# Performance work log

Measured on AMD Instinct MI355X. Metric: run time of the kernel, lower is better.

The kernel has to match this reference:

```python
import jax, jax.numpy as jnp
import numpy as np

N = 100000      # number of nodes (z rows) and z0 rows
E = 1000000     # number of edges
EMB = 128       # args.emb_size


def setup_inputs() -> dict:
    key = jax.random.key(0)
    k1, k2, k3, k4, k5 = jax.random.split(key, 5)
    z = jax.random.normal(k1, (N, EMB), dtype=jnp.float32)
    z0 = jax.random.normal(k2, (N, EMB), dtype=jnp.float32)
    edge_index = jax.random.randint(k3, (2, E), 0, N, dtype=jnp.int64)
    # torch Linear weights: [out_features, in_features]
    Wq = jax.random.normal(k4, (EMB, 2 * EMB), dtype=jnp.float32) * (1.0 / np.sqrt(2 * EMB))
    Wo = jax.random.normal(k5, (1, 2 * EMB), dtype=jnp.float32) * (1.0 / np.sqrt(2 * EMB))
    bo = jnp.zeros((1,), dtype=jnp.float32)
    return {"z": z, "edge_index": edge_index, "z0": z0, "Wq": Wq, "Wo": Wo, "bo": bo}


def reference(z, edge_index, z0, Wq, Wo, bo):
    # qid: per-edge max of the two endpoint ids, shifted to start at 0
    qid = jnp.max(edge_index[0:2], axis=0)
    qid = qid - qid.min()
    emb1 = z[edge_index[0]]            # [E, EMB]
    emb2 = z[edge_index[1]]            # [E, EMB]
    x0 = jnp.concatenate([emb2, z0[qid]], axis=-1) @ Wq.T   # [E, EMB]
    out = jnp.concatenate([emb1, x0], axis=-1) @ Wo.T + bo  # [E, 1]
    return out.reshape(-1)
```

## Files before the change

kernel.cpp:

```cpp
#include <hip/hip_runtime.h>
#include <climits>

#define EMB 128
#define EMB2 256

__global__ void prep_weights_kernel(const float* __restrict__ Wq,
                                    const float* __restrict__ Wo,
                                    float* __restrict__ weff,
                                    int* __restrict__ qmin) {
    int k = threadIdx.x;
    float acc = 0.f;
#pragma unroll 8
    for (int j = 0; j < EMB; ++j)
        acc += Wo[EMB + j] * Wq[j * EMB2 + k];
    weff[k] = acc;
    if (k == 0) *qmin = INT_MAX;
}

__global__ void qmin_kernel(const int* __restrict__ ei, int E,
                            int* __restrict__ qmin) {
    int m = INT_MAX;
    int nvec = E >> 2;
    int stride = gridDim.x * blockDim.x;
    const int4* r0 = (const int4*)ei;
    const int4* r1 = (const int4*)(ei + E);
    for (int v = blockIdx.x * blockDim.x + threadIdx.x; v < nvec; v += stride) {
        int4 a = r0[v];
        int4 b = r1[v];
        int m0 = max(a.x, b.x), m1 = max(a.y, b.y);
        int m2 = max(a.z, b.z), m3 = max(a.w, b.w);
        m = min(m, min(min(m0, m1), min(m2, m3)));
    }
    if (blockIdx.x == 0 && threadIdx.x < (E & 3)) {
        int e = (nvec << 2) + threadIdx.x;
        m = min(m, max(ei[e], ei[e + E]));
    }
    for (int off = 32; off; off >>= 1)
        m = min(m, __shfl_xor(m, off, 64));
    __shared__ int sm[8];
    int wid = threadIdx.x >> 6;
    if ((threadIdx.x & 63) == 0) sm[wid] = m;
    __syncthreads();
    if (threadIdx.x == 0) {
        int nw = blockDim.x >> 6;
        int r = sm[0];
        for (int w = 1; w < nw; ++w) r = min(r, sm[w]);
        atomicMin(qmin, r);
    }
}

__global__ void node_dots_kernel(const float* __restrict__ z,
                                 const float* __restrict__ z0,
                                 const float* __restrict__ Wo,
                                 const float* __restrict__ weff,
                                 float4* __restrict__ tab,
                                 int N) {
    int gtid = blockIdx.x * blockDim.x + threadIdx.x;
    int wave = gtid >> 6;
    int lane = gtid & 63;
    int sub = lane >> 5;
    int c = lane & 31;
    int row = wave * 2 + sub;
    if (row >= N) return;

    float4 w1 = ((const float4*)Wo)[c];
    float4 wa = ((const float4*)weff)[c];
    float4 wb = ((const float4*)weff)[32 + c];

    float4 zv  = ((const float4*)(z  + (size_t)row * EMB))[c];
    float4 z0v = ((const float4*)(z0 + (size_t)row * EMB))[c];

    float p1 = w1.x * zv.x + w1.y * zv.y + w1.z * zv.z + w1.w * zv.w;
    float p2 = wa.x * zv.x + wa.y * zv.y + wa.z * zv.z + wa.w * zv.w;
    float p3 = wb.x * z0v.x + wb.y * z0v.y + wb.z * z0v.z + wb.w * z0v.w;

#pragma unroll
    for (int off = 16; off; off >>= 1) {
        p1 += __shfl_xor(p1, off, 64);
        p2 += __shfl_xor(p2, off, 64);
        p3 += __shfl_xor(p3, off, 64);
    }
    if (c == 0) tab[row] = make_float4(p1, p2, p3, 0.f);
}

__global__ void edge_out_kernel(const int* __restrict__ ei,
                                const float4* __restrict__ tab,
                                const int* __restrict__ qminp,
                                const float* __restrict__ bo,
                                float* __restrict__ out, int E) {
    int qmin = *qminp;
    float b0 = *bo;
    int t = blockIdx.x * blockDim.x + threadIdx.x;
    int e4 = t << 2;
    if (e4 + 3 < E) {
        int4 a = *(const int4*)(ei + e4);
        int4 b = *(const int4*)(ei + E + e4);
        float4 r;
        r.x = tab[a.x].x + tab[b.x].y + tab[max(a.x, b.x) - qmin].z + b0;
        r.y = tab[a.y].x + tab[b.y].y + tab[max(a.y, b.y) - qmin].z + b0;
        r.z = tab[a.z].x + tab[b.z].y + tab[max(a.z, b.z) - qmin].z + b0;
        r.w = tab[a.w].x + tab[b.w].y + tab[max(a.w, b.w) - qmin].z + b0;
        *(float4*)(out + e4) = r;
    } else {
        for (int e = e4; e < E; ++e) {
            int a = ei[e], b = ei[e + E];
            out[e] = tab[a].x + tab[b].y + tab[max(a, b) - qmin].z + b0;
        }
    }
}

extern "C" void kernel_launch(void* const* d_in, const int* in_sizes, int n_in,
                              void* d_out, int out_size, void* d_ws, size_t ws_size,
                              hipStream_t stream) {
    const float* z    = (const float*)d_in[0];
    const int*   ei   = (const int*)d_in[1];
    const float* z0   = (const float*)d_in[2];
    const float* Wq   = (const float*)d_in[3];
    const float* Wo   = (const float*)d_in[4];
    const float* bo   = (const float*)d_in[5];
    float* out = (float*)d_out;

    int N = in_sizes[0] / EMB;
    int E = in_sizes[1] / 2;

    float4* tab = (float4*)d_ws;
    float* weff = (float*)(tab + N);
    int*   qmin = (int*)(weff + EMB2);

    prep_weights_kernel<<<1, EMB2, 0, stream>>>(Wq, Wo, weff, qmin);

    qmin_kernel<<<512, 256, 0, stream>>>(ei, E, qmin);

    int pairs = (N + 1) / 2;
    int blocksC = (pairs + 3) / 4;
    node_dots_kernel<<<blocksC, 256, 0, stream>>>(z, z0, Wo, weff, tab, N);

    int threadsD = (E + 3) / 4;
    int blocksD = (threadsD + 255) / 256;
    edge_out_kernel<<<blocksD, 256, 0, stream>>>(ei, tab, qmin, bo, out, E);
}
```

Measured before the change: 158.6 us.

## Fuse qid-min scan into node dot-product kernel and use nontemporal loads/stores

```diff
diff --git a/kernel.cpp b/kernel.cpp
--- a/kernel.cpp
+++ b/kernel.cpp
@@ -4,10 +4,13 @@
 #define EMB 128
 #define EMB2 256
 
-__global__ void prep_weights_kernel(const float* __restrict__ Wq,
-                                    const float* __restrict__ Wo,
-                                    float* __restrict__ weff,
-                                    int* __restrict__ qmin) {
+typedef float v4f __attribute__((ext_vector_type(4)));
+typedef int   v4i __attribute__((ext_vector_type(4)));
+
+__global__ void weff_kernel(const float* __restrict__ Wq,
+                            const float* __restrict__ Wo,
+                            float* __restrict__ weff,
+                            int* __restrict__ qmin) {
     int k = threadIdx.x;
     float acc = 0.f;
 #pragma unroll 8
@@ -17,74 +20,78 @@
     if (k == 0) *qmin = INT_MAX;
 }
 
-__global__ void qmin_kernel(const int* __restrict__ ei, int E,
-                            int* __restrict__ qmin) {
-    int m = INT_MAX;
-    int nvec = E >> 2;
-    int stride = gridDim.x * blockDim.x;
-    const int4* r0 = (const int4*)ei;
-    const int4* r1 = (const int4*)(ei + E);
-    for (int v = blockIdx.x * blockDim.x + threadIdx.x; v < nvec; v += stride) {
-        int4 a = r0[v];
-        int4 b = r1[v];
-        int m0 = max(a.x, b.x), m1 = max(a.y, b.y);
-        int m2 = max(a.z, b.z), m3 = max(a.w, b.w);
-        m = min(m, min(min(m0, m1), min(m2, m3)));
-    }
-    if (blockIdx.x == 0 && threadIdx.x < (E & 3)) {
-        int e = (nvec << 2) + threadIdx.x;
-        m = min(m, max(ei[e], ei[e + E]));
-    }
-    for (int off = 32; off; off >>= 1)
-        m = min(m, __shfl_xor(m, off, 64));
-    __shared__ int sm[8];
-    int wid = threadIdx.x >> 6;
-    if ((threadIdx.x & 63) == 0) sm[wid] = m;
-    __syncthreads();
-    if (threadIdx.x == 0) {
-        int nw = blockDim.x >> 6;
-        int r = sm[0];
-        for (int w = 1; w < nw; ++w) r = min(r, sm[w]);
-        atomicMin(qmin, r);
-    }
-}
-
-__global__ void node_dots_kernel(const float* __restrict__ z,
+__global__ void scan_dots_kernel(const float* __restrict__ z,
                                  const float* __restrict__ z0,
+                                 const int* __restrict__ ei, int E,
                                  const float* __restrict__ Wo,
                                  const float* __restrict__ weff,
-                                 float4* __restrict__ tab,
-                                 int N) {
-    int gtid = blockIdx.x * blockDim.x + threadIdx.x;
-    int wave = gtid >> 6;
-    int lane = gtid & 63;
-    int sub = lane >> 5;
-    int c = lane & 31;
-    int row = wave * 2 + sub;
+                                 v4f* __restrict__ tab, int N,
+                                 int* __restrict__ qmin) {
+    const int gtid = blockIdx.x * blockDim.x + threadIdx.x;
+
+    {
+        int m = INT_MAX;
+        const int nvec = E >> 2;
+        if (gtid < nvec) {
+            v4i a = ((const v4i*)ei)[gtid];
+            v4i b = ((const v4i*)(ei + E))[gtid];
+            int m0 = max(a.x, b.x), m1 = max(a.y, b.y);
+            int m2 = max(a.z, b.z), m3 = max(a.w, b.w);
+            m = min(min(m0, m1), min(m2, m3));
+        }
+        if (gtid < (E & 3)) {
+            int e = (nvec << 2) + gtid;
+            m = min(m, max(ei[e], ei[e + E]));
+        }
+#pragma unroll
+        for (int off = 32; off; off >>= 1)
+            m = min(m, __shfl_xor(m, off, 64));
+        __shared__ int sm[4];
+        if ((threadIdx.x & 63) == 0) sm[threadIdx.x >> 6] = m;
+        __syncthreads();
+        if (threadIdx.x == 0)
+            atomicMin(qmin, min(min(sm[0], sm[1]), min(sm[2], sm[3])));
+    }
+
+    const int wave = gtid >> 6;
+    const int lane = gtid & 63;
+    const int sub = lane >> 4;
+    const int c = lane & 15;
+    const int row = wave * 4 + sub;
     if (row >= N) return;
 
-    float4 w1 = ((const float4*)Wo)[c];
-    float4 wa = ((const float4*)weff)[c];
-    float4 wb = ((const float4*)weff)[32 + c];
+    v4f w1a = ((const v4f*)Wo)[c],        w1b = ((const v4f*)Wo)[16 + c];
+    v4f waa = ((const v4f*)weff)[c],      wab = ((const v4f*)weff)[16 + c];
+    v4f wba = ((const v4f*)weff)[32 + c], wbb = ((const v4f*)weff)[48 + c];
 
-    float4 zv  = ((const float4*)(z  + (size_t)row * EMB))[c];
-    float4 z0v = ((const float4*)(z0 + (size_t)row * EMB))[c];
+    const v4f* zr  = (const v4f*)(z  + (size_t)row * EMB);
+    const v4f* z0r = (const v4f*)(z0 + (size_t)row * EMB);
+    v4f za = __builtin_nontemporal_load(zr + c);
+    v4f zb = __builtin_nontemporal_load(zr + 16 + c);
+    v4f qa = __builtin_nontemporal_load(z0r + c);
+    v4f qb = __builtin_nontemporal_load(z0r + 16 + c);
 
-    float p1 = w1.x * zv.x + w1.y * zv.y + w1.z * zv.z + w1.w * zv.w;
-    float p2 = wa.x * zv.x + wa.y * zv.y + wa.z * zv.z + wa.w * zv.w;
-    float p3 = wb.x * z0v.x + wb.y * z0v.y + wb.z * z0v.z + wb.w * z0v.w;
+    float p1 = w1a.x * za.x + w1a.y * za.y + w1a.z * za.z + w1a.w * za.w
+             + w1b.x * zb.x + w1b.y * zb.y + w1b.z * zb.z + w1b.w * zb.w;
+    float p2 = waa.x * za.x + waa.y * za.y + waa.z * za.z + waa.w * za.w
+             + wab.x * zb.x + wab.y * zb.y + wab.z * zb.z + wab.w * zb.w;
+    float p3 = wba.x * qa.x + wba.y * qa.y + wba.z * qa.z + wba.w * qa.w
+             + wbb.x * qb.x + wbb.y * qb.y + wbb.z * qb.z + wbb.w * qb.w;
 
 #pragma unroll
-    for (int off = 16; off; off >>= 1) {
+    for (int off = 8; off; off >>= 1) {
         p1 += __shfl_xor(p1, off, 64);
         p2 += __shfl_xor(p2, off, 64);
         p3 += __shfl_xor(p3, off, 64);
     }
-    if (c == 0) tab[row] = make_float4(p1, p2, p3, 0.f);
+    if (c == 0) {
+        v4f r; r.x = p1; r.y = p2; r.z = p3; r.w = 0.f;
+        tab[row] = r;
+    }
 }
 
 __global__ void edge_out_kernel(const int* __restrict__ ei,
-                                const float4* __restrict__ tab,
+                                const v4f* __restrict__ tab,
                                 const int* __restrict__ qminp,
                                 const float* __restrict__ bo,
                                 float* __restrict__ out, int E) {
@@ -93,14 +100,14 @@
     int t = blockIdx.x * blockDim.x + threadIdx.x;
     int e4 = t << 2;
     if (e4 + 3 < E) {
-        int4 a = *(const int4*)(ei + e4);
-        int4 b = *(const int4*)(ei + E + e4);
-        float4 r;
+        v4i a = *(const v4i*)(ei + e4);
+        v4i b = *(const v4i*)(ei + E + e4);
+        v4f r;
         r.x = tab[a.x].x + tab[b.x].y + tab[max(a.x, b.x) - qmin].z + b0;
         r.y = tab[a.y].x + tab[b.y].y + tab[max(a.y, b.y) - qmin].z + b0;
         r.z = tab[a.z].x + tab[b.z].y + tab[max(a.z, b.z) - qmin].z + b0;
         r.w = tab[a.w].x + tab[b.w].y + tab[max(a.w, b.w) - qmin].z + b0;
-        *(float4*)(out + e4) = r;
+        __builtin_nontemporal_store(r, (v4f*)(out + e4));
     } else {
         for (int e = e4; e < E; ++e) {
             int a = ei[e], b = ei[e + E];
@@ -123,19 +130,19 @@
     int N = in_sizes[0] / EMB;
     int E = in_sizes[1] / 2;
 
-    float4* tab = (float4*)d_ws;
+    v4f*  tab   = (v4f*)d_ws;
     float* weff = (float*)(tab + N);
-    int*   qmin = (int*)(weff + EMB2);
+    int*  qmin  = (int*)(weff + EMB2);
 
-    prep_weights_kernel<<<1, EMB2, 0, stream>>>(Wq, Wo, weff, qmin);
+    weff_kernel<<<1, EMB2, 0, stream>>>(Wq, Wo, weff, qmin);
 
-    qmin_kernel<<<512, 256, 0, stream>>>(ei, E, qmin);
+    int wavesB = (N + 3) / 4;
+    int blocksB = (wavesB + 3) / 4;
+    int blocksScan = ((E + 3) / 4 + 255) / 256;
+    int blocks2 = blocksB > blocksScan ? blocksB : blocksScan;
+    scan_dots_kernel<<<blocks2, 256, 0, stream>>>(z, z0, ei, E, Wo, weff,
+                                                  tab, N, qmin);
 
-    int pairs = (N + 1) / 2;
-    int blocksC = (pairs + 3) / 4;
-    node_dots_kernel<<<blocksC, 256, 0, stream>>>(z, z0, Wo, weff, tab, N);
-
-    int threadsD = (E + 3) / 4;
-    int blocksD = (threadsD + 255) / 256;
+    int blocksD = ((E + 3) / 4 + 255) / 256;
     edge_out_kernel<<<blocksD, 256, 0, stream>>>(ei, tab, qmin, bo, out, E);
 }
```

Measured after the change: 211.2 us. +33.2%, slower.
